# Performance work log

Measured on AMD Instinct MI355X. Metric: run time of the kernel, lower is better.

The kernel has to match this reference:

```python
import jax, jax.numpy as jnp
import numpy as np

IMG = 224
PS = 2
C_IN = 3
EMBED = 768
BATCH = 256
SLICES = IMG // 2            # 112
L = 2 * (SLICES // PS)       # 112 levels
K = IMG * PS                 # 448 gathered (a,b) pairs per level
D_IN = K * C_IN              # 1344


def _build_levels(n=IMG, slices=SLICES, ps=PS):
    """Replicates LUnraveling index construction (natural order; set() in the
    original only permutes within a level, which is equivalent up to a fixed
    permutation of weight columns for random init)."""
    a_list, b_list = [], []
    ar = np.arange(n)
    for i in range(slices // ps):
        cols = range(i * ps, (i + 1) * ps)
        # 'up' level: pairs (j, col) for j in range(n), concatenated over ps cols
        a_list.append(np.concatenate([ar for _ in cols]))
        b_list.append(np.concatenate([np.full(n, c) for c in cols]))
        # 'right' level: pairs (n - slices + col, j) for j in range(n)
        a_list.append(np.concatenate([np.full(n, n - slices + c) for c in cols]))
        b_list.append(np.concatenate([ar for _ in cols]))
    return (np.stack(a_list).astype(np.int32), np.stack(b_list).astype(np.int32))


def setup_inputs() -> dict:
    key = jax.random.key(0)
    k1, k2, k3 = jax.random.split(key, 3)
    x = jax.random.normal(k1, (BATCH, C_IN, IMG, IMG), dtype=jnp.float32)
    W = jax.random.normal(k2, (EMBED, D_IN), dtype=jnp.float32) * (1.0 / np.sqrt(D_IN))
    b = jax.random.normal(k3, (EMBED,), dtype=jnp.float32) * 0.01
    a_np, b_np = _build_levels()
    return {"x": x, "W": W, "b": b,
            "a_idx": jnp.asarray(a_np), "b_idx": jnp.asarray(b_np)}


def reference(x, W, b, a_idx, b_idx):
    B = x.shape[0]
    # gather: x[:, :, a, b] with (L,K) index arrays -> (B, C, L, K)
    g = x[:, :, a_idx, b_idx]
    # per-level flatten(1) in torch flattens (C, K) C-major -> (B, L, C*K)
    g = jnp.transpose(g, (0, 2, 1, 3)).reshape(B, L, C_IN * K)
    # shared linear projection per level token
    tokens = jnp.einsum('bld,ed->ble', g, W) + b
    return tokens  # (B, L, EMBED); norm is Identity (norm_layer=None)
```

## Files before the change

kernel.cpp:

```cpp
#include <hip/hip_runtime.h>
#include <stdint.h>


#define IMG   224
#define NLEV  112
#define CIN   3
#define DIN   1344
#define EMB   768
#define BATCH 256
#define MTOT  28672

#define BM    128
#define BN    128
#define BK    64
#define LDP   72

#define AS1 __attribute__((address_space(1)))
#define AS3 __attribute__((address_space(3)))

typedef __attribute__((ext_vector_type(8))) short   short8;
typedef __attribute__((ext_vector_type(4))) float   floatx4;

__device__ __forceinline__ unsigned short f2bf(float f) {
    unsigned u = __float_as_uint(f);
    unsigned r = (u + 0x7fffu + ((u >> 16) & 1u)) >> 16;
    return (unsigned short)r;
}
__device__ __forceinline__ float bf2f(unsigned short s) {
    return __uint_as_float(((unsigned)s) << 16);
}
__device__ __forceinline__ unsigned pack2(float a, float b) {
    return (unsigned)f2bf(a) | ((unsigned)f2bf(b) << 16);
}

__global__ void detect_dtype(const unsigned short* __restrict__ W, int* flag) {
    __shared__ int s;
    if (threadIdx.x == 0) s = 0;
    __syncthreads();
    int bad = 0;
    for (int k = threadIdx.x; k < 4096; k += 256) {
        unsigned v = (unsigned)W[2 * k] & 0x7FFFu;
        if (v >= 0x4000u) bad = 1;
    }
    if (bad) atomicOr(&s, 1);
    __syncthreads();
    if (threadIdx.x == 0) *flag = s;
}

template<bool F32>
__global__ __launch_bounds__(256)
void pack_w(const void* __restrict__ Wv, const void* __restrict__ Bv,
            unsigned short* __restrict__ Wb, float* __restrict__ Bf,
            const int* __restrict__ flag)
{
    if (*flag != (F32 ? 1 : 0)) return;
    const int idx = blockIdx.x * 256 + threadIdx.x;
    if (F32) {
        const float4* s = (const float4*)((const float*)Wv + (size_t)idx * 8);
        float4 x0 = s[0], x1 = s[1];
        uint4 o;
        o.x = pack2(x0.x, x0.y); o.y = pack2(x0.z, x0.w);
        o.z = pack2(x1.x, x1.y); o.w = pack2(x1.z, x1.w);
        ((uint4*)Wb)[idx] = o;
    } else {
        ((uint4*)Wb)[idx] = ((const uint4*)Wv)[idx];
    }
    if (idx < EMB)
        Bf[idx] = F32 ? ((const float*)Bv)[idx]
                      : bf2f(((const unsigned short*)Bv)[idx]);
}

template<bool F32>
__global__ __launch_bounds__(256)
void pack_g(const void* __restrict__ Xv, unsigned short* __restrict__ Gc,
            int b0, const int* __restrict__ flag)
{
    if (*flag != (F32 ? 1 : 0)) return;
    __shared__ __align__(16) unsigned short lds[IMG * 116];

    const int tid = threadIdx.x;
    const int bl  = blockIdx.x;
    const int b   = b0 + bl;
    const int c   = blockIdx.y;
    const size_t plane = ((size_t)b * CIN + c) * (size_t)(IMG * IMG);
    unsigned short* Grow = Gc + (size_t)bl * NLEV * DIN + (size_t)c * 448;

    if (F32) {
        const float* src = (const float*)Xv + plane + (size_t)NLEV * IMG;
        for (int v = tid; v < 3136; v += 256) {
            const int i  = v / 56;
            const int kk = (v - i * 56) * 8;
            const float4* s = (const float4*)(src + (size_t)v * 8);
            float4 x0 = s[0], x1 = s[1];
            uint4 o;
            o.x = pack2(x0.x, x0.y); o.y = pack2(x0.z, x0.w);
            o.z = pack2(x1.x, x1.y); o.w = pack2(x1.z, x1.w);
            *(uint4*)(Grow + (size_t)(2 * i + 1) * DIN + kk) = o;
        }
    } else {
        const unsigned short* src = (const unsigned short*)Xv + plane + (size_t)NLEV * IMG;
        for (int v = tid; v < 3136; v += 256) {
            const int i  = v / 56;
            const int kk = (v - i * 56) * 8;
            *(uint4*)(Grow + (size_t)(2 * i + 1) * DIN + kk) =
                *(const uint4*)(src + (size_t)v * 8);
        }
    }

    for (int v = tid; v < 3136; v += 256) {
        const int r  = v / 14;
        const int vv = v - r * 14;
        if (F32) {
            const float4* s = (const float4*)((const float*)Xv + plane
                              + (size_t)r * IMG + (size_t)vv * 8);
            float4 x0 = s[0], x1 = s[1];
            uint2 o0, o1;
            o0.x = pack2(x0.x, x0.y); o0.y = pack2(x0.z, x0.w);
            o1.x = pack2(x1.x, x1.y); o1.y = pack2(x1.z, x1.w);
            *(uint2*)&lds[r * 116 + vv * 8]     = o0;
            *(uint2*)&lds[r * 116 + vv * 8 + 4] = o1;
        } else {
            const uint2* s = (const uint2*)((const unsigned short*)Xv + plane
                              + (size_t)r * IMG + (size_t)vv * 8);
            *(uint2*)&lds[r * 116 + vv * 8]     = s[0];
            *(uint2*)&lds[r * 116 + vv * 8 + 4] = s[1];
        }
    }
    __syncthreads();
    for (int idx = tid; idx < 56 * IMG; idx += 256) {
        const int pr = idx / IMG;
        const int r  = idx - pr * IMG;
        const unsigned v = *(const unsigned*)&lds[r * 116 + 2 * pr];
        unsigned short* dst = Grow + (size_t)(2 * pr) * DIN + r;
        dst[0]   = (unsigned short)(v & 0xFFFFu);
        dst[IMG] = (unsigned short)(v >> 16);
    }
}

__global__ __launch_bounds__(256)
void gemm_packed(const unsigned short* __restrict__ G,
                 const unsigned short* __restrict__ Wb,
                 const float* __restrict__ Bf,
                 float* __restrict__ Out)
{
    __shared__ __align__(16) unsigned short As[128 * 64];
    __shared__ __align__(16) unsigned short Bs[128 * 64];

    const int tid   = threadIdx.x;
    const int wave  = tid >> 6;
    const int lane  = tid & 63;
    const int mBase = blockIdx.x * 128;
    const int nBase = blockIdx.y * 128;
    const int wm    = wave >> 1, wn = wave & 1;
    const int lrow  = lane & 15;
    const int kq    = (lane >> 4) << 3;

    floatx4 acc[4][4];
    #pragma unroll
    for (int i = 0; i < 4; i++)
        #pragma unroll
        for (int j = 0; j < 4; j++)
            acc[i][j] = (floatx4){0.f, 0.f, 0.f, 0.f};

    const unsigned short* gaP[4];
    const unsigned short* gbP[4];
    unsigned ldsOff[4];
    #pragma unroll
    for (int i = 0; i < 4; i++) {
        const int idx = (i * 4 + wave) * 64 + lane;
        const int row = idx >> 3, k8 = idx & 7;
        gaP[i] = G  + (size_t)(mBase + row) * DIN + k8 * 8;
        gbP[i] = Wb + (size_t)(nBase + row) * DIN + k8 * 8;
        ldsOff[i] = (unsigned)((i * 4 + wave) * 512);
    }

    for (int kt = 0; kt < DIN; kt += 64) {
        #pragma unroll
        for (int i = 0; i < 4; i++) {
            __builtin_amdgcn_global_load_lds(
                (const AS1 void*)(gaP[i] + kt),
                (AS3 void*)(As + ldsOff[i]), 16, 0, 0);
            __builtin_amdgcn_global_load_lds(
                (const AS1 void*)(gbP[i] + kt),
                (AS3 void*)(Bs + ldsOff[i]), 16, 0, 0);
        }
        __syncthreads();

        #pragma unroll
        for (int k0 = 0; k0 < 64; k0 += 32) {
            short8 af[4], bfv[4];
            #pragma unroll
            for (int mi = 0; mi < 4; mi++)
                af[mi] = *(const short8*)&As[(wm * 64 + mi * 16 + lrow) * 64 + k0 + kq];
            #pragma unroll
            for (int ni = 0; ni < 4; ni++)
                bfv[ni] = *(const short8*)&Bs[(wn * 64 + ni * 16 + lrow) * 64 + k0 + kq];
            #pragma unroll
            for (int mi = 0; mi < 4; mi++)
                #pragma unroll
                for (int ni = 0; ni < 4; ni++)
                    acc[mi][ni] = __builtin_amdgcn_mfma_f32_16x16x32_bf16(
                        af[mi], bfv[ni], acc[mi][ni], 0, 0, 0);
        }
        __syncthreads();
    }

    const int quad = lane >> 4;
    #pragma unroll
    for (int ni = 0; ni < 4; ni++) {
        const int col = nBase + wn * 64 + ni * 16 + lrow;
        const float bv = Bf[col];
        #pragma unroll
        for (int mi = 0; mi < 4; mi++) {
            const int rbase = mBase + wm * 64 + mi * 16 + quad * 4;
            floatx4 a = acc[mi][ni];
            Out[(size_t)(rbase + 0) * EMB + col] = a[0] + bv;
            Out[(size_t)(rbase + 1) * EMB + col] = a[1] + bv;
            Out[(size_t)(rbase + 2) * EMB + col] = a[2] + bv;
            Out[(size_t)(rbase + 3) * EMB + col] = a[3] + bv;
        }
    }
}

template<bool F32>
__global__ __launch_bounds__(256, 2)
void lfreq_fused_gemm(const void* __restrict__ Xv,
                      const void* __restrict__ Wv,
                      const void* __restrict__ Bv,
                      const int* __restrict__ Aidx,
                      const int* __restrict__ Bidx,
                      float* __restrict__ Out,
                      const int* __restrict__ flag)
{
    if (*flag != (F32 ? 1 : 0)) return;

    __shared__ __align__(16) unsigned short As[BM][LDP];
    __shared__ __align__(16) unsigned short Bs[BN][LDP];

    const int tid   = threadIdx.x;
    const int wave  = tid >> 6;
    const int lane  = tid & 63;
    const int mBase = blockIdx.x * BM;
    const int nBase = blockIdx.y * BN;

    const int srow  = tid >> 1;
    const int shalf = tid & 1;
    const int am = mBase + srow;
    const int bb = am / NLEV;
    const int ll = am - bb * NLEV;

    floatx4 acc[4][4];
    #pragma unroll
    for (int i = 0; i < 4; i++)
        #pragma unroll
        for (int jj = 0; jj < 4; jj++)
            acc[i][jj] = (floatx4){0.f, 0.f, 0.f, 0.f};

    const int wm   = wave >> 1;
    const int wn   = wave & 1;
    const int lrow = lane & 15;
    const int kq   = (lane >> 4) << 3;

    for (int kt = 0; kt < DIN; kt += BK) {
        {
            const int koff = kt + shalf * 32;
            uint4* dst = (uint4*)&Bs[srow][shalf * 32];
            if (F32) {
                const float4* g = (const float4*)((const float*)Wv
                                + (size_t)(nBase + srow) * DIN + koff);
                #pragma unroll
                for (int q = 0; q < 4; q++) {
                    float4 v0 = g[2*q], v1 = g[2*q+1];
                    uint4 o;
                    o.x = pack2(v0.x, v0.y); o.y = pack2(v0.z, v0.w);
                    o.z = pack2(v1.x, v1.y); o.w = pack2(v1.z, v1.w);
                    dst[q] = o;
                }
            } else {
                const uint4* g = (const uint4*)((const unsigned short*)Wv
                               + (size_t)(nBase + srow) * DIN + koff);
                #pragma unroll
                for (int q = 0; q < 4; q++) dst[q] = g[q];
            }
        }
        {
            const int d0  = kt + shalf * 32;
            const int c   = (d0 >= 896) ? 2 : (d0 >= 448 ? 1 : 0);
            const int kk0 = d0 - c * 448;
            const int4* ap = (const int4*)(Aidx + ll * 448 + kk0);
            const int4* bp = (const int4*)(Bidx + ll * 448 + kk0);
            unsigned* du = (unsigned*)&As[srow][shalf * 32];
            if (F32) {
                const float* plane = (const float*)Xv
                    + (size_t)bb * (CIN * IMG * IMG) + (size_t)c * (IMG * IMG);
                #pragma unroll
                for (int q = 0; q < 8; q++) {
                    int4 av = ap[q], bv = bp[q];
                    du[2*q+0] = pack2(plane[av.x * IMG + bv.x], plane[av.y * IMG + bv.y]);
                    du[2*q+1] = pack2(plane[av.z * IMG + bv.z], plane[av.w * IMG + bv.w]);
                }
            } else {
                const unsigned short* plane = (const unsigned short*)Xv
                    + (size_t)bb * (CIN * IMG * IMG) + (size_t)c * (IMG * IMG);
                #pragma unroll
                for (int q = 0; q < 8; q++) {
                    int4 av = ap[q], bv = bp[q];
                    unsigned e0 = plane[av.x * IMG + bv.x];
                    unsigned e1 = plane[av.y * IMG + bv.y];
                    unsigned e2 = plane[av.z * IMG + bv.z];
                    unsigned e3 = plane[av.w * IMG + bv.w];
                    du[2*q+0] = e0 | (e1 << 16);
                    du[2*q+1] = e2 | (e3 << 16);
                }
            }
        }
        __syncthreads();

        #pragma unroll
        for (int k0 = 0; k0 < BK; k0 += 32) {
            short8 af[4], bfv[4];
            #pragma unroll
            for (int mi = 0; mi < 4; mi++)
                af[mi] = *(const short8*)&As[wm*64 + mi*16 + lrow][k0 + kq];
            #pragma unroll
            for (int ni = 0; ni < 4; ni++)
                bfv[ni] = *(const short8*)&Bs[wn*64 + ni*16 + lrow][k0 + kq];
            #pragma unroll
            for (int mi = 0; mi < 4; mi++)
                #pragma unroll
                for (int ni = 0; ni < 4; ni++)
                    acc[mi][ni] = __builtin_amdgcn_mfma_f32_16x16x32_bf16(
                        af[mi], bfv[ni], acc[mi][ni], 0, 0, 0);
        }
        __syncthreads();
    }

    const int quad = lane >> 4;
    #pragma unroll
    for (int ni = 0; ni < 4; ni++) {
        const int col = nBase + wn*64 + ni*16 + lrow;
        const float bv = F32 ? ((const float*)Bv)[col]
                             : bf2f(((const unsigned short*)Bv)[col]);
        #pragma unroll
        for (int mi = 0; mi < 4; mi++) {
            const int rbase = mBase + wm*64 + mi*16 + quad*4;
            floatx4 a = acc[mi][ni];
            Out[(size_t)(rbase+0)*EMB + col] = a[0] + bv;
            Out[(size_t)(rbase+1)*EMB + col] = a[1] + bv;
            Out[(size_t)(rbase+2)*EMB + col] = a[2] + bv;
            Out[(size_t)(rbase+3)*EMB + col] = a[3] + bv;
        }
    }
}

extern "C" void kernel_launch(void* const* d_in, const int* in_sizes, int n_in,
                              void* d_out, int out_size, void* d_ws, size_t ws_size,
                              hipStream_t stream) {
    const void* X    = d_in[0];
    const void* Wt   = d_in[1];
    const void* Bias = d_in[2];
    const int*  Ai   = (const int*)d_in[3];
    const int*  Bi   = (const int*)d_in[4];
    float* Out = (float*)d_out;

    char* ws  = (char*)d_ws;
    int* flag = (int*)ws;

    detect_dtype<<<dim3(1), dim3(256), 0, stream>>>((const unsigned short*)Wt, flag);

    float* Bf          = (float*)(ws + 256);
    unsigned short* Wb = (unsigned short*)(ws + 4096);
    const size_t gOff  = 4096 + (size_t)EMB * DIN * 2;
    unsigned short* Gc = (unsigned short*)(ws + gOff);

    int CHB = 0;
    const int cand[6] = {256, 128, 64, 32, 16, 8};
    for (int t = 0; t < 6; t++) {
        if (gOff + (size_t)cand[t] * NLEV * DIN * 2 <= ws_size) { CHB = cand[t]; break; }
    }

    if (CHB == 0) {
        dim3 grid(MTOT / BM, EMB / BN);
        lfreq_fused_gemm<false><<<grid, dim3(256), 0, stream>>>(X, Wt, Bias, Ai, Bi, Out, flag);
        lfreq_fused_gemm<true ><<<grid, dim3(256), 0, stream>>>(X, Wt, Bias, Ai, Bi, Out, flag);
        return;
    }

    pack_w<false><<<dim3(504), dim3(256), 0, stream>>>(Wt, Bias, Wb, Bf, flag);
    pack_w<true ><<<dim3(504), dim3(256), 0, stream>>>(Wt, Bias, Wb, Bf, flag);

    for (int b0 = 0; b0 < BATCH; b0 += CHB) {
        dim3 pgrid(CHB, CIN);
        pack_g<false><<<pgrid, dim3(256), 0, stream>>>(X, Gc, b0, flag);
        pack_g<true ><<<pgrid, dim3(256), 0, stream>>>(X, Gc, b0, flag);
        dim3 ggrid(CHB * NLEV / 128, EMB / 128);
        gemm_packed<<<ggrid, dim3(256), 0, stream>>>(Gc, Wb, Bf,
                                                     Out + (size_t)b0 * NLEV * EMB);
    }
}
```

Measured before the change: 369.3 us.

## Merge dtype-templated packers, split gather into row/col kernels, vectorize stores, XCD-remap GEMM

The packing kernels no longer come in two dtype-templated copies that each exit early. They now branch on the runtime flag inside a single kernel, which removes one launch per stage. The gather is split into a row-copy kernel and an LDS-transpose column kernel. The column kernel now packs 8 rows per thread and writes 16-byte vector stores instead of scattered 2-byte stores. The GEMM uses a 1D grid with an XCD-aware block-index remap so that neighbouring tiles share an XCD's L2, at the cost of some index arithmetic.

```diff
diff --git a/kernel.cpp b/kernel.cpp
--- a/kernel.cpp
+++ b/kernel.cpp
@@ -47,13 +47,12 @@
     if (threadIdx.x == 0) *flag = s;
 }
 
-template<bool F32>
 __global__ __launch_bounds__(256)
 void pack_w(const void* __restrict__ Wv, const void* __restrict__ Bv,
             unsigned short* __restrict__ Wb, float* __restrict__ Bf,
             const int* __restrict__ flag)
 {
-    if (*flag != (F32 ? 1 : 0)) return;
+    const bool F32 = (*flag != 0);
     const int idx = blockIdx.x * 256 + threadIdx.x;
     if (F32) {
         const float4* s = (const float4*)((const float*)Wv + (size_t)idx * 8);
@@ -70,19 +69,15 @@
                       : bf2f(((const unsigned short*)Bv)[idx]);
 }
 
-template<bool F32>
 __global__ __launch_bounds__(256)
-void pack_g(const void* __restrict__ Xv, unsigned short* __restrict__ Gc,
-            int b0, const int* __restrict__ flag)
+void pack_g_rows(const void* __restrict__ Xv, unsigned short* __restrict__ Gc,
+                 int b0, const int* __restrict__ flag)
 {
-    if (*flag != (F32 ? 1 : 0)) return;
-    __shared__ __align__(16) unsigned short lds[IMG * 116];
-
+    const bool F32 = (*flag != 0);
     const int tid = threadIdx.x;
     const int bl  = blockIdx.x;
-    const int b   = b0 + bl;
     const int c   = blockIdx.y;
-    const size_t plane = ((size_t)b * CIN + c) * (size_t)(IMG * IMG);
+    const size_t plane = ((size_t)(b0 + bl) * CIN + c) * (size_t)(IMG * IMG);
     unsigned short* Grow = Gc + (size_t)bl * NLEV * DIN + (size_t)c * 448;
 
     if (F32) {
@@ -106,6 +101,20 @@
                 *(const uint4*)(src + (size_t)v * 8);
         }
     }
+}
+
+__global__ __launch_bounds__(256)
+void pack_g_cols(const void* __restrict__ Xv, unsigned short* __restrict__ Gc,
+                 int b0, const int* __restrict__ flag)
+{
+    const bool F32 = (*flag != 0);
+    __shared__ __align__(16) unsigned short lds[IMG * 116];
+
+    const int tid = threadIdx.x;
+    const int bl  = blockIdx.x;
+    const int c   = blockIdx.y;
+    const size_t plane = ((size_t)(b0 + bl) * CIN + c) * (size_t)(IMG * IMG);
+    unsigned short* Grow = Gc + (size_t)bl * NLEV * DIN + (size_t)c * 448;
 
     for (int v = tid; v < 3136; v += 256) {
         const int r  = v / 14;
@@ -127,13 +136,27 @@
         }
     }
     __syncthreads();
-    for (int idx = tid; idx < 56 * IMG; idx += 256) {
-        const int pr = idx / IMG;
-        const int r  = idx - pr * IMG;
-        const unsigned v = *(const unsigned*)&lds[r * 116 + 2 * pr];
-        unsigned short* dst = Grow + (size_t)(2 * pr) * DIN + r;
-        dst[0]   = (unsigned short)(v & 0xFFFFu);
-        dst[IMG] = (unsigned short)(v >> 16);
+
+    for (int idx = tid; idx < 56 * 28; idx += 256) {
+        const int pr = idx / 28;
+        const int t  = idx - pr * 28;
+        const int r0 = t * 8;
+        unsigned v[8];
+        #pragma unroll
+        for (int j = 0; j < 8; j++)
+            v[j] = *(const unsigned*)&lds[(r0 + j) * 116 + 2 * pr];
+        uint4 lo, hi;
+        lo.x = (v[0] & 0xFFFFu) | (v[1] << 16);
+        lo.y = (v[2] & 0xFFFFu) | (v[3] << 16);
+        lo.z = (v[4] & 0xFFFFu) | (v[5] << 16);
+        lo.w = (v[6] & 0xFFFFu) | (v[7] << 16);
+        hi.x = (v[0] >> 16) | (v[1] & 0xFFFF0000u);
+        hi.y = (v[2] >> 16) | (v[3] & 0xFFFF0000u);
+        hi.z = (v[4] >> 16) | (v[5] & 0xFFFF0000u);
+        hi.w = (v[6] >> 16) | (v[7] & 0xFFFF0000u);
+        unsigned short* dst = Grow + (size_t)(2 * pr) * DIN + r0;
+        *(uint4*)dst         = lo;
+        *(uint4*)(dst + IMG) = hi;
     }
 }
 
@@ -146,14 +169,23 @@
     __shared__ __align__(16) unsigned short As[128 * 64];
     __shared__ __align__(16) unsigned short Bs[128 * 64];
 
-    const int tid   = threadIdx.x;
-    const int wave  = tid >> 6;
-    const int lane  = tid & 63;
-    const int mBase = blockIdx.x * 128;
-    const int nBase = blockIdx.y * 128;
-    const int wm    = wave >> 1, wn = wave & 1;
-    const int lrow  = lane & 15;
-    const int kq    = (lane >> 4) << 3;
+    const int tid  = threadIdx.x;
+    const int wave = tid >> 6;
+    const int lane = tid & 63;
+
+    const int bid = blockIdx.x;
+    const int nwg = gridDim.x;
+    const int q = nwg >> 3, r = nwg & 7;
+    const int xcd = bid & 7, s = bid >> 3;
+    const int lid = (xcd < r ? xcd * (q + 1) : r * (q + 1) + (xcd - r) * q) + s;
+    const int mT = lid / 6;
+    const int nT = lid - mT * 6;
+    const int mBase = mT * 128;
+    const int nBase = nT * 128;
+
+    const int wm   = wave >> 1, wn = wave & 1;
+    const int lrow = lane & 15;
+    const int kq   = (lane >> 4) << 3;
 
     floatx4 acc[4][4];
     #pragma unroll
@@ -386,14 +418,13 @@
         return;
     }
 
-    pack_w<false><<<dim3(504), dim3(256), 0, stream>>>(Wt, Bias, Wb, Bf, flag);
-    pack_w<true ><<<dim3(504), dim3(256), 0, stream>>>(Wt, Bias, Wb, Bf, flag);
+    pack_w<<<dim3(504), dim3(256), 0, stream>>>(Wt, Bias, Wb, Bf, flag);
 
     for (int b0 = 0; b0 < BATCH; b0 += CHB) {
         dim3 pgrid(CHB, CIN);
-        pack_g<false><<<pgrid, dim3(256), 0, stream>>>(X, Gc, b0, flag);
-        pack_g<true ><<<pgrid, dim3(256), 0, stream>>>(X, Gc, b0, flag);
-        dim3 ggrid(CHB * NLEV / 128, EMB / 128);
+        pack_g_rows<<<pgrid, dim3(256), 0, stream>>>(X, Gc, b0, flag);
+        pack_g_cols<<<pgrid, dim3(256), 0, stream>>>(X, Gc, b0, flag);
+        dim3 ggrid(CHB * NLEV / 128 * 6);
         gemm_packed<<<ggrid, dim3(256), 0, stream>>>(Gc, Wb, Bf,
                                                      Out + (size_t)b0 * NLEV * EMB);
     }
```

New measurement: 363.9 us. No clear change (-1.5%).
